# Performance work log

Measured on AMD Instinct MI355X. Metric: run time of the kernel, lower is better.

The kernel has to match this reference:

```python
import jax, jax.numpy as jnp
import numpy as np

# ---- layer config (yolov3, layer_no=2) ----
STRIDE = 8
N_CLASSES = 80
IGNORE_TH = 0.7
ANCHORS_PX = np.array([[10,13],[16,30],[33,23],[30,61],[62,45],[59,119],[116,90],[156,198],[373,326]], np.float32)
ALL_ANCHORS = ANCHORS_PX / STRIDE          # [9,2] in grid units
ANCHOR_ID_LO, ANCHOR_ID_HI = 0, 2          # anchor_mask[2] = [0,1,2]
ANCHORS = ALL_ANCHORS[ANCHOR_ID_LO:ANCHOR_ID_HI+1]  # [3,2]
NA = 3
NC = N_CLASSES + 5

B, IN_CH, NG, NBOX = 16, 256, 76, 50


def _safe_log(p):
    # emulate torch BCE's log clamp at -100; eps stops 0*inf -> nan
    return jnp.maximum(jnp.log(jnp.maximum(p, 1e-12)), -100.0)


def _bce_sum(p, t, w=None):
    l = -(t * _safe_log(p) + (1.0 - t) * _safe_log(1.0 - p))
    if w is not None:
        l = l * w
    return l.sum()


def setup_inputs() -> dict:
    key = jax.random.key(0)
    k1, k2, k3, k4, k5 = jax.random.split(key, 5)
    xin = jax.random.normal(k1, (B, IN_CH, NG, NG), jnp.float32)
    cls = jax.random.randint(k2, (B, NBOX, 1), 0, N_CLASSES).astype(jnp.float32)
    cxy = jax.random.uniform(k3, (B, NBOX, 2), jnp.float32, 0.02, 0.98)
    wh = jax.random.uniform(k4, (B, NBOX, 2), jnp.float32, 0.02, 0.40)
    labels = jnp.concatenate([cls, cxy, wh], axis=-1)  # [B,N,5]
    W = jax.random.normal(k5, (NA * NC, IN_CH), jnp.float32) * 0.02  # 1x1 conv
    b = jnp.zeros((NA * NC,), jnp.float32)
    return {"xin": xin, "labels": labels, "W": W, "b": b}


def _yolo_loss(xin, labels, W, b):
    nB, _, nG, _ = xin.shape
    anchors = jnp.asarray(ANCHORS, xin.dtype)          # [3,2]
    all_anchors = jnp.asarray(ALL_ANCHORS, xin.dtype)  # [9,2]

    # 1x1 conv -> [B, A, G, G, C]
    x = jnp.einsum('bchw,oc->bohw', xin, W) + b[None, :, None, None]
    x = x.reshape(nB, NA, NC, nG, nG).transpose(0, 1, 3, 4, 2)

    xy = jax.nn.sigmoid(x[..., :2])
    wh = x[..., 2:4]
    conf_cls = jax.nn.sigmoid(x[..., 4:])  # [B,A,G,G,1+ncls]

    gy, gx = jnp.meshgrid(jnp.arange(nG, dtype=x.dtype), jnp.arange(nG, dtype=x.dtype), indexing='ij')
    pred_boxes = jnp.stack([
        xy[..., 0] + gx,
        xy[..., 1] + gy,
        jnp.exp(wh[..., 0]) * anchors[:, 0][None, :, None, None],
        jnp.exp(wh[..., 1]) * anchors[:, 1][None, :, None, None]], axis=-1)  # [B,A,G,G,4]

    # ---- ground truth ----
    valid = labels.sum(-1) > 0                     # [B,N]
    gt_cls = labels[..., 0].astype(jnp.int32)
    gt = labels[..., 1:] * nG                      # [B,N,4] cx,cy,w,h in grid units
    gt_x, gt_y, gt_w, gt_h = gt[..., 0], gt[..., 1], gt[..., 2], gt[..., 3]
    gi = jnp.floor(gt_x).astype(jnp.int32)
    gj = jnp.floor(gt_y).astype(jnp.int32)

    # best anchor per gt: wh-IoU vs all 9 anchors (centered at origin)
    inter_a = jnp.minimum(gt_w[..., None], all_anchors[:, 0]) * jnp.minimum(gt_h[..., None], all_anchors[:, 1])
    union_a = gt_w[..., None] * gt_h[..., None] + all_anchors[:, 0] * all_anchors[:, 1] - inter_a
    best = jnp.argmax(inter_a / union_a, axis=-1)  # [B,N]
    in_mask = (best >= ANCHOR_ID_LO) & (best <= ANCHOR_ID_HI)
    a = jnp.where(in_mask, best % 3, -1)           # [B,N]

    # all-pairs IoU: pred boxes vs gt boxes (ignore mask)
    pb = pred_boxes.reshape(nB, -1, 4)             # [B,M,4], M = A*G*G
    pa_area = pb[..., 2] * pb[..., 3]
    gt_area = gt_w * gt_h
    tl = jnp.maximum(pb[:, :, None, :2] - pb[:, :, None, 2:] / 2, gt[:, None, :, :2] - gt[:, None, :, 2:] / 2)
    br = jnp.minimum(pb[:, :, None, :2] + pb[:, :, None, 2:] / 2, gt[:, None, :, :2] + gt[:, None, :, 2:] / 2)
    inter = jnp.prod(br - tl, -1) * jnp.all(tl < br, -1)
    iou = inter / (pa_area[:, :, None] + gt_area[:, None, :] - inter)
    iou = jnp.where(valid[:, None, :], iou, 0.0)
    best_iou = iou.max(-1)                         # [B,M]
    has_boxes = valid.any(-1)
    obj_mask = jnp.where(has_boxes[:, None], best_iou <= IGNORE_TH, True).reshape(nB, NA, nG, nG)

    # ---- scatter target assignment ----
    assign = valid & (a >= 0)
    a_safe = jnp.clip(a, 0, NA - 1)
    aw = anchors[a_safe, 0]
    ah = anchors[a_safe, 1]
    tvec = jnp.concatenate([
        (gt_x - jnp.floor(gt_x))[..., None],
        (gt_y - jnp.floor(gt_y))[..., None],
        jnp.log(gt_w / aw + 1e-16)[..., None],
        jnp.log(gt_h / ah + 1e-16)[..., None],
        jnp.ones_like(gt_x)[..., None],
        jax.nn.one_hot(gt_cls, N_CLASSES, dtype=x.dtype)], axis=-1)  # [B,N,NC]
    sval = 2.0 - gt_w * gt_h / (nG * nG)

    bf = jnp.broadcast_to(jnp.arange(nB)[:, None], a.shape).reshape(-1)
    af = jnp.where(assign, a_safe, NA).reshape(-1)  # NA is OOB -> dropped
    jf = gj.reshape(-1)
    if_ = gi.reshape(-1)

    target = jnp.zeros((nB, NA, nG, nG, NC), x.dtype).at[bf, af, jf, if_].set(tvec.reshape(-1, NC), mode='drop')
    scale = jnp.zeros((nB, NA, nG, nG), x.dtype).at[bf, af, jf, if_].set(sval.reshape(-1), mode='drop')
    obj_mask = obj_mask.at[bf, af, jf, if_].set(True, mode='drop')
    noobj = jnp.zeros((nB, NA, nG, nG), bool).at[bf, af, jf, if_].set(True, mode='drop')

    # ---- losses ----
    nm = noobj.astype(x.dtype)[..., None]
    p_obj = conf_cls[..., 0] * obj_mask
    t_obj = target[..., 4] * obj_mask
    p_xy = xy * nm
    t_xy = target[..., :2] * nm
    p_wh = wh * nm
    t_wh = target[..., 2:4] * nm
    p_cls = conf_cls[..., 1:] * nm
    t_cls = target[..., 5:] * nm
    sc = scale[..., None]

    loss_xy = _bce_sum(p_xy, t_xy, sc)
    rs = jnp.sqrt(sc)
    loss_wh = 0.5 * jnp.sum((p_wh * rs - t_wh * rs) ** 2)
    loss_obj = _bce_sum(p_obj, t_obj)
    loss_cls = _bce_sum(p_cls, t_cls)
    loss = loss_xy + loss_wh + loss_obj + loss_cls
    return jnp.stack([loss, loss_xy, loss_wh, loss_obj, loss_cls])


def reference(xin, labels, W, b):
    return _yolo_loss(xin, labels, W, b)
```

## Files before the change

### kernel.cpp

```cpp
#include <hip/hip_runtime.h>
#include <math.h>

#define NB    16
#define NAg   3
#define NCg   85
#define NCLS  80
#define NGg   76
#define NSp   (NGg*NGg)
#define NBOX  50
#define INCH  256
#define SPB   256
#define GBLK  ((NSp + SPB - 1) / SPB)
#define GXDIM (GBLK + NBOX)
#define TOTBLK (GXDIM * NB)

#define ACC_OFF  0
#define HAS_OFF  32
#define DONE_OFF 96
#define WT_OFF   128
#define GB_OFF   (WT_OFF + 16384)
#define GA_OFF   (GB_OFF + 25600)
#define GI_OFF   (GA_OFF + 25600)

__device__ __constant__ float c_AW[9] = {1.25f,2.0f,4.125f,3.75f,7.75f,7.375f,14.5f,19.5f,46.625f};
__device__ __constant__ float c_AH[9] = {1.625f,3.75f,2.875f,7.625f,5.625f,14.875f,11.25f,24.75f,40.75f};

__device__ __forceinline__ float safe_log(float p) {
    return fmaxf(logf(fmaxf(p, 1e-12f)), -100.0f);
}
__device__ __forceinline__ float sigm(float x) {
    return 1.0f / (1.0f + expf(-x));
}

__global__ __launch_bounds__(256) void k_labels(
    const float* __restrict__ labels, const float* __restrict__ W,
    float* __restrict__ Wt, float* __restrict__ gbox, float* __restrict__ gaux,
    int* __restrict__ gint, int* __restrict__ hasAny, float* __restrict__ acc,
    int* __restrict__ done)
{
    const int b = blockIdx.x, tid = threadIdx.x;
    const int t = b * 256 + tid;

    {
        const int c = t >> 4, f = t & 15;
        Wt[t] = (f < 15) ? W[((f / 5) * NCg + (f % 5)) * INCH + c] : 0.f;
    }
    if (b == 0 && tid < 8)  acc[tid] = 0.f;
    if (b == 0 && tid == 8) *done = 0;

    int valid = 0;
    if (tid < NBOX) {
        const int bt = b * NBOX + tid;
        const float* L = labels + (size_t)bt * 5;
        const float l0 = L[0], l1 = L[1], l2 = L[2], l3 = L[3], l4 = L[4];
        valid = (l0 + l1 + l2 + l3 + l4) > 0.f;

        const float gx = l1 * NGg, gy = l2 * NGg, gw = l3 * NGg, gh = l4 * NGg;

        int best = 0; float brr = -1.f;
#pragma unroll
        for (int k = 0; k < 9; k++) {
            float inter = fminf(gw, c_AW[k]) * fminf(gh, c_AH[k]);
            float uni   = gw*gh + c_AW[k]*c_AH[k] - inter;
            float r     = inter / uni;
            if (r > brr) { brr = r; best = k; }
        }
        const int a = (best <= 2) ? best : -1;
        const int assign = valid && (a >= 0);
        const int a_safe = a < 0 ? 0 : (a > 2 ? 2 : a);

        const int gi = (int)floorf(gx), gj = (int)floorf(gy);
        const int inb = (gi >= 0) && (gi < NGg) && (gj >= 0) && (gj < NGg);
        const int cell = (assign && inb) ? (a * NSp + gj * NGg + gi) : -1;

        float* gb = gbox + (size_t)bt * 8;
        gb[0] = gx - gw * 0.5f;
        gb[1] = gy - gh * 0.5f;
        gb[2] = gx + gw * 0.5f;
        gb[3] = gy + gh * 0.5f;
        gb[4] = valid ? gw * gh : -1.f;
        gb[5] = __int_as_float(cell);

        float* ga = gaux + (size_t)bt * 8;
        ga[0] = gx - floorf(gx);
        ga[1] = gy - floorf(gy);
        ga[2] = logf(gw / c_AW[a_safe] + 1e-16f);
        ga[3] = logf(gh / c_AH[a_safe] + 1e-16f);
        ga[4] = 2.f - gw * gh / (float)NSp;

        gint[bt*2 + 0] = cell;
        gint[bt*2 + 1] = (int)l0;
    }
    if (tid < 64) {
        const unsigned long long m = __ballot(valid != 0);
        if (tid == 0) hasAny[b] = (m != 0ULL) ? 1 : 0;
    }
}

__global__ __launch_bounds__(256) void k_mega(
    const float* __restrict__ xin, const float* __restrict__ Wt,
    const float* __restrict__ W, const float* __restrict__ bias,
    const float* __restrict__ gbox, const float* __restrict__ gaux,
    const int* __restrict__ gint, const int* __restrict__ hasAny,
    float* __restrict__ acc, int* __restrict__ done, float* __restrict__ out)
{
    __shared__ __align__(16) float smem[15364];

    const int bx  = blockIdx.x;
    const int b   = blockIdx.y;
    const int tid = threadIdx.x;

    if (bx < GBLK) {
        float (*part)[15][SPB] = (float (*)[15][SPB])smem;
        float* wred = smem + 4 * 15 * SPB;

        const int w  = tid >> 6, l = tid & 63;
        const int wu = __builtin_amdgcn_readfirstlane(w);
        const int pb = bx * SPB;

        float4 ac[15];
#pragma unroll
        for (int f = 0; f < 15; ++f) ac[f] = make_float4(0.f,0.f,0.f,0.f);

        const float* xp = xin + ((size_t)b * INCH + (wu << 6)) * NSp + pb + 4*l;
        const float* wp = Wt + ((wu << 6) << 4);

        if (pb + SPB <= NSp) {
            for (int c0 = 0; c0 < 64; c0 += 8) {
                float4 v[8];
#pragma unroll
                for (int k = 0; k < 8; ++k)
                    v[k] = *(const float4*)(xp + (size_t)(c0 + k) * NSp);
#pragma unroll
                for (int k = 0; k < 8; ++k) {
                    const float* wr = wp + ((c0 + k) << 4);
#pragma unroll
                    for (int f = 0; f < 15; ++f) {
                        const float wv = wr[f];
                        ac[f].x += wv * v[k].x;  ac[f].y += wv * v[k].y;
                        ac[f].z += wv * v[k].z;  ac[f].w += wv * v[k].w;
                    }
                }
            }
        } else {
            const bool lv = (pb + 4*l) < NSp;
            const float4 z = make_float4(0.f,0.f,0.f,0.f);
            for (int c0 = 0; c0 < 64; c0 += 8) {
                float4 v[8];
#pragma unroll
                for (int k = 0; k < 8; ++k)
                    v[k] = lv ? *(const float4*)(xp + (size_t)(c0 + k) * NSp) : z;
#pragma unroll
                for (int k = 0; k < 8; ++k) {
                    const float* wr = wp + ((c0 + k) << 4);
#pragma unroll
                    for (int f = 0; f < 15; ++f) {
                        const float wv = wr[f];
                        ac[f].x += wv * v[k].x;  ac[f].y += wv * v[k].y;
                        ac[f].z += wv * v[k].z;  ac[f].w += wv * v[k].w;
                    }
                }
            }
        }

#pragma unroll
        for (int f = 0; f < 15; ++f)
            *(float4*)&part[w][f][4*l] = ac[f];
        __syncthreads();

        float lsum = 0.f;
        const int p = pb + tid;
        if (p < NSp) {
            float xv[15];
#pragma unroll
            for (int f = 0; f < 15; ++f)
                xv[f] = part[0][f][tid] + part[1][f][tid]
                      + part[2][f][tid] + part[3][f][tid];

            const int sy = p / NGg;
            const int sx = p - sy * NGg;
            const float gxf = (float)sx, gyf = (float)sy;

            float pbx0[3], pby0[3], pbx1[3], pby1[3], pa[3], cf[3];
#pragma unroll
            for (int a = 0; a < 3; ++a) {
                const float px = sigm(xv[a*5+0] + bias[a*NCg+0]) + gxf;
                const float py = sigm(xv[a*5+1] + bias[a*NCg+1]) + gyf;
                const float pw = expf(xv[a*5+2] + bias[a*NCg+2]) * c_AW[a];
                const float ph = expf(xv[a*5+3] + bias[a*NCg+3]) * c_AH[a];
                cf[a]   = sigm(xv[a*5+4] + bias[a*NCg+4]);
                pbx0[a] = px - pw * 0.5f;  pby0[a] = py - ph * 0.5f;
                pbx1[a] = px + pw * 0.5f;  pby1[a] = py + ph * 0.5f;
                pa[a]   = pw * ph;
            }

            int mask = 0;
            const float* gb = gbox + (size_t)b * NBOX * 8;
            for (int n = 0; n < NBOX; ++n) {
                const float bx0 = gb[n*8+0], by0 = gb[n*8+1];
                const float bx1 = gb[n*8+2], by1 = gb[n*8+3];
                const float gar = gb[n*8+4];
                const int cell  = __float_as_int(gb[n*8+5]);
                const int d = cell - p;
                if (d == 0)       mask |= 8;
                if (d == NSp)     mask |= 16;
                if (d == 2*NSp)   mask |= 32;
                if (gar >= 0.f) {
#pragma unroll
                    for (int a = 0; a < 3; ++a) {
                        const float tlx = fmaxf(pbx0[a], bx0);
                        const float tly = fmaxf(pby0[a], by0);
                        const float brx = fminf(pbx1[a], bx1);
                        const float bry = fminf(pby1[a], by1);
                        const float dx = brx - tlx, dy = bry - tly;
                        const float inter = (dx > 0.f && dy > 0.f) ? dx * dy : 0.f;
                        if (inter > 0.7f * (pa[a] + gar - inter)) mask |= (1 << a);
                    }
                }
            }

            const bool hasB = hasAny[b] != 0;
#pragma unroll
            for (int a = 0; a < 3; ++a) {
                const bool ex = (mask & (1 << a)) != 0;
                const bool as = (mask & (8 << a)) != 0;
                const bool maskpre = hasB ? (!ex) : true;
                if (maskpre || as) {
                    const float c = cf[a];
                    lsum += as ? -safe_log(c) : -safe_log(1.f - c);
                }
            }
        }

#pragma unroll
        for (int off = 32; off > 0; off >>= 1) lsum += __shfl_down(lsum, off);
        if ((tid & 63) == 0) wred[tid >> 6] = lsum;
        __syncthreads();
        if (tid == 0) atomicAdd(&acc[2], wred[0] + wred[1] + wred[2] + wred[3]);

    } else {
        int*    scell = (int*)smem;
        float4* col4  = (float4*)(smem + 64);
        float*  xsh   = smem + 64 + 256;
        float*  sacc  = smem + 64 + 256 + 96;

        const int n = bx - GBLK;
        const int t = b * NBOX + n;

        if (tid < NBOX) scell[tid] = gint[(b * NBOX + tid) * 2];
        __syncthreads();

        const int cell = scell[n];
        bool win = (cell >= 0);
        if (win)
            for (int n2 = n + 1; n2 < NBOX; ++n2)
                if (scell[n2] == cell) { win = false; break; }

        if (win) {
            const int a = cell / NSp, s = cell % NSp;
            const int o0 = a * NCg;

            ((float*)col4)[tid] = xin[((size_t)b * INCH + tid) * NSp + s];
            if (tid < 3) sacc[tid] = 0.f;
            __syncthreads();

            const int wid = tid >> 6, lane = tid & 63;
            for (int o = wid; o < NCg; o += 4) {
                const float4 wv = *(const float4*)&W[(size_t)(o0 + o) * INCH + lane * 4];
                const float4 cv = col4[lane];
                float p = wv.x*cv.x + wv.y*cv.y + wv.z*cv.z + wv.w*cv.w;
                for (int off = 32; off; off >>= 1) p += __shfl_down(p, off);
                if (lane == 0) xsh[o] = p + bias[o0 + o];
            }
            __syncthreads();

            if (tid < NCg) {
                const float* ga = gaux + (size_t)t * 8;
                const float sval = ga[4];
                const int gcls = gint[t*2 + 1];
                float val = xsh[tid];
                float term; int slot;
                if (tid < 2) {
                    float tgt = ga[tid];
                    float p = sigm(val);
                    term = -(tgt * safe_log(p) + (1.f - tgt) * safe_log(1.f - p)) * sval;
                    slot = 0;
                } else if (tid < 4) {
                    float tgt = ga[tid];
                    float d = val - tgt;
                    term = 0.5f * sval * d * d;
                    slot = 1;
                } else if (tid == 4) {
                    term = 0.f; slot = 2;
                } else {
                    float tgt = ((tid - 5) == gcls) ? 1.f : 0.f;
                    float p = sigm(val);
                    term = -(tgt * safe_log(p) + (1.f - tgt) * safe_log(1.f - p));
                    slot = 2;
                }
                atomicAdd(&sacc[slot], term);
            }
            __syncthreads();
            if (tid == 0) {
                atomicAdd(&acc[0], sacc[0]);
                atomicAdd(&acc[1], sacc[1]);
                atomicAdd(&acc[3], sacc[2]);
            }
        }
    }

    __syncthreads();
    if (tid == 0) {
        __threadfence();
        const int v = atomicAdd(done, 1);
        if (v == TOTBLK - 1) {
            const float xy = atomicAdd(&acc[0], 0.f);
            const float wh = atomicAdd(&acc[1], 0.f);
            const float ob = atomicAdd(&acc[2], 0.f);
            const float cl = atomicAdd(&acc[3], 0.f);
            out[0] = xy + wh + ob + cl;
            out[1] = xy; out[2] = wh; out[3] = ob; out[4] = cl;
        }
    }
}

extern "C" void kernel_launch(void* const* d_in, const int* in_sizes, int n_in,
                              void* d_out, int out_size, void* d_ws, size_t ws_size,
                              hipStream_t stream)
{
    const float* xin    = (const float*)d_in[0];
    const float* labels = (const float*)d_in[1];
    const float* W      = (const float*)d_in[2];
    const float* bias   = (const float*)d_in[3];

    char* ws = (char*)d_ws;
    float* acc    = (float*)(ws + ACC_OFF);
    int*   hasAny = (int*)  (ws + HAS_OFF);
    int*   done   = (int*)  (ws + DONE_OFF);
    float* Wt     = (float*)(ws + WT_OFF);
    float* gbox   = (float*)(ws + GB_OFF);
    float* gaux   = (float*)(ws + GA_OFF);
    int*   gint   = (int*)  (ws + GI_OFF);
    float* out    = (float*)d_out;

    k_labels<<<16, 256, 0, stream>>>(labels, W, Wt, gbox, gaux, gint, hasAny, acc, done);

    k_mega<<<dim3(GXDIM, NB), 256, 0, stream>>>(xin, Wt, W, bias, gbox, gaux,
                                                gint, hasAny, acc, done, out);
}
```

Measured before the change: 205.2 us.

## Fold per-box target blocks into spatial blocks via strided loop

Removes the 50 extra per-GT-box blocks per batch from the grid. Each spatial conv/objectness block now also handles a strided subset of the GT boxes after its main work, reusing its shared memory. This shrinks the grid and the completion-counter traffic, but adds serial per-box work and extra barriers to the tail of the spatial blocks.

Measured after the change: 196.6 us. 1.04x faster.

```diff
diff --git a/kernel.cpp b/kernel.cpp
--- a/kernel.cpp
+++ b/kernel.cpp
@@ -11,8 +11,7 @@
 #define INCH  256
 #define SPB   256
 #define GBLK  ((NSp + SPB - 1) / SPB)
-#define GXDIM (GBLK + NBOX)
-#define TOTBLK (GXDIM * NB)
+#define TOTBLK (GBLK * NB)
 
 #define ACC_OFF  0
 #define HAS_OFF  32
@@ -97,159 +96,152 @@
     }
 }
 
-__global__ __launch_bounds__(256) void k_mega(
+__global__ __launch_bounds__(256) void k_main(
     const float* __restrict__ xin, const float* __restrict__ Wt,
     const float* __restrict__ W, const float* __restrict__ bias,
     const float* __restrict__ gbox, const float* __restrict__ gaux,
     const int* __restrict__ gint, const int* __restrict__ hasAny,
     float* __restrict__ acc, int* __restrict__ done, float* __restrict__ out)
 {
-    __shared__ __align__(16) float smem[15364];
+    __shared__ float part[4][15][SPB];
+    __shared__ float wred[4];
 
     const int bx  = blockIdx.x;
     const int b   = blockIdx.y;
     const int tid = threadIdx.x;
-
-    if (bx < GBLK) {
-        float (*part)[15][SPB] = (float (*)[15][SPB])smem;
-        float* wred = smem + 4 * 15 * SPB;
-
-        const int w  = tid >> 6, l = tid & 63;
-        const int wu = __builtin_amdgcn_readfirstlane(w);
-        const int pb = bx * SPB;
-
-        float4 ac[15];
-#pragma unroll
-        for (int f = 0; f < 15; ++f) ac[f] = make_float4(0.f,0.f,0.f,0.f);
-
-        const float* xp = xin + ((size_t)b * INCH + (wu << 6)) * NSp + pb + 4*l;
-        const float* wp = Wt + ((wu << 6) << 4);
-
-        if (pb + SPB <= NSp) {
-            for (int c0 = 0; c0 < 64; c0 += 8) {
-                float4 v[8];
-#pragma unroll
-                for (int k = 0; k < 8; ++k)
-                    v[k] = *(const float4*)(xp + (size_t)(c0 + k) * NSp);
-#pragma unroll
-                for (int k = 0; k < 8; ++k) {
-                    const float* wr = wp + ((c0 + k) << 4);
-#pragma unroll
-                    for (int f = 0; f < 15; ++f) {
-                        const float wv = wr[f];
-                        ac[f].x += wv * v[k].x;  ac[f].y += wv * v[k].y;
-                        ac[f].z += wv * v[k].z;  ac[f].w += wv * v[k].w;
-                    }
+    const int w   = tid >> 6, l = tid & 63;
+    const int wu  = __builtin_amdgcn_readfirstlane(w);
+    const int pb  = bx * SPB;
+
+    float4 ac[15];
+#pragma unroll
+    for (int f = 0; f < 15; ++f) ac[f] = make_float4(0.f,0.f,0.f,0.f);
+
+    const float* xp = xin + ((size_t)b * INCH + (wu << 6)) * NSp + pb + 4*l;
+    const float* wp = Wt + ((wu << 6) << 4);
+
+    if (pb + SPB <= NSp) {
+        for (int c0 = 0; c0 < 64; c0 += 8) {
+            float4 v[8];
+#pragma unroll
+            for (int k = 0; k < 8; ++k)
+                v[k] = *(const float4*)(xp + (size_t)(c0 + k) * NSp);
+#pragma unroll
+            for (int k = 0; k < 8; ++k) {
+                const float* wr = wp + ((c0 + k) << 4);
+#pragma unroll
+                for (int f = 0; f < 15; ++f) {
+                    const float wv = wr[f];
+                    ac[f].x += wv * v[k].x;  ac[f].y += wv * v[k].y;
+                    ac[f].z += wv * v[k].z;  ac[f].w += wv * v[k].w;
                 }
             }
-        } else {
-            const bool lv = (pb + 4*l) < NSp;
-            const float4 z = make_float4(0.f,0.f,0.f,0.f);
-            for (int c0 = 0; c0 < 64; c0 += 8) {
-                float4 v[8];
-#pragma unroll
-                for (int k = 0; k < 8; ++k)
-                    v[k] = lv ? *(const float4*)(xp + (size_t)(c0 + k) * NSp) : z;
-#pragma unroll
-                for (int k = 0; k < 8; ++k) {
-                    const float* wr = wp + ((c0 + k) << 4);
-#pragma unroll
-                    for (int f = 0; f < 15; ++f) {
-                        const float wv = wr[f];
-                        ac[f].x += wv * v[k].x;  ac[f].y += wv * v[k].y;
-                        ac[f].z += wv * v[k].z;  ac[f].w += wv * v[k].w;
-                    }
+        }
+    } else {
+        const bool lv = (pb + 4*l) < NSp;
+        const float4 z = make_float4(0.f,0.f,0.f,0.f);
+        for (int c0 = 0; c0 < 64; c0 += 8) {
+            float4 v[8];
+#pragma unroll
+            for (int k = 0; k < 8; ++k)
+                v[k] = lv ? *(const float4*)(xp + (size_t)(c0 + k) * NSp) : z;
+#pragma unroll
+            for (int k = 0; k < 8; ++k) {
+                const float* wr = wp + ((c0 + k) << 4);
+#pragma unroll
+                for (int f = 0; f < 15; ++f) {
+                    const float wv = wr[f];
+                    ac[f].x += wv * v[k].x;  ac[f].y += wv * v[k].y;
+                    ac[f].z += wv * v[k].z;  ac[f].w += wv * v[k].w;
                 }
             }
         }
-
+    }
+
+#pragma unroll
+    for (int f = 0; f < 15; ++f)
+        *(float4*)&part[w][f][4*l] = ac[f];
+    __syncthreads();
+
+    float lsum = 0.f;
+    const int p = pb + tid;
+    if (p < NSp) {
+        float xv[15];
 #pragma unroll
         for (int f = 0; f < 15; ++f)
-            *(float4*)&part[w][f][4*l] = ac[f];
-        __syncthreads();
-
-        float lsum = 0.f;
-        const int p = pb + tid;
-        if (p < NSp) {
-            float xv[15];
-#pragma unroll
-            for (int f = 0; f < 15; ++f)
-                xv[f] = part[0][f][tid] + part[1][f][tid]
-                      + part[2][f][tid] + part[3][f][tid];
-
-            const int sy = p / NGg;
-            const int sx = p - sy * NGg;
-            const float gxf = (float)sx, gyf = (float)sy;
-
-            float pbx0[3], pby0[3], pbx1[3], pby1[3], pa[3], cf[3];
-#pragma unroll
-            for (int a = 0; a < 3; ++a) {
-                const float px = sigm(xv[a*5+0] + bias[a*NCg+0]) + gxf;
-                const float py = sigm(xv[a*5+1] + bias[a*NCg+1]) + gyf;
-                const float pw = expf(xv[a*5+2] + bias[a*NCg+2]) * c_AW[a];
-                const float ph = expf(xv[a*5+3] + bias[a*NCg+3]) * c_AH[a];
-                cf[a]   = sigm(xv[a*5+4] + bias[a*NCg+4]);
-                pbx0[a] = px - pw * 0.5f;  pby0[a] = py - ph * 0.5f;
-                pbx1[a] = px + pw * 0.5f;  pby1[a] = py + ph * 0.5f;
-                pa[a]   = pw * ph;
-            }
-
-            int mask = 0;
-            const float* gb = gbox + (size_t)b * NBOX * 8;
-            for (int n = 0; n < NBOX; ++n) {
-                const float bx0 = gb[n*8+0], by0 = gb[n*8+1];
-                const float bx1 = gb[n*8+2], by1 = gb[n*8+3];
-                const float gar = gb[n*8+4];
-                const int cell  = __float_as_int(gb[n*8+5]);
-                const int d = cell - p;
-                if (d == 0)       mask |= 8;
-                if (d == NSp)     mask |= 16;
-                if (d == 2*NSp)   mask |= 32;
-                if (gar >= 0.f) {
-#pragma unroll
-                    for (int a = 0; a < 3; ++a) {
-                        const float tlx = fmaxf(pbx0[a], bx0);
-                        const float tly = fmaxf(pby0[a], by0);
-                        const float brx = fminf(pbx1[a], bx1);
-                        const float bry = fminf(pby1[a], by1);
-                        const float dx = brx - tlx, dy = bry - tly;
-                        const float inter = (dx > 0.f && dy > 0.f) ? dx * dy : 0.f;
-                        if (inter > 0.7f * (pa[a] + gar - inter)) mask |= (1 << a);
-                    }
+            xv[f] = part[0][f][tid] + part[1][f][tid]
+                  + part[2][f][tid] + part[3][f][tid];
+
+        const int sy = p / NGg;
+        const int sx = p - sy * NGg;
+        const float gxf = (float)sx, gyf = (float)sy;
+
+        float pbx0[3], pby0[3], pbx1[3], pby1[3], pa[3], cf[3];
+#pragma unroll
+        for (int a = 0; a < 3; ++a) {
+            const float px = sigm(xv[a*5+0] + bias[a*NCg+0]) + gxf;
+            const float py = sigm(xv[a*5+1] + bias[a*NCg+1]) + gyf;
+            const float pw = expf(xv[a*5+2] + bias[a*NCg+2]) * c_AW[a];
+            const float ph = expf(xv[a*5+3] + bias[a*NCg+3]) * c_AH[a];
+            cf[a]   = sigm(xv[a*5+4] + bias[a*NCg+4]);
+            pbx0[a] = px - pw * 0.5f;  pby0[a] = py - ph * 0.5f;
+            pbx1[a] = px + pw * 0.5f;  pby1[a] = py + ph * 0.5f;
+            pa[a]   = pw * ph;
+        }
+
+        int mask = 0;
+        const float* gb = gbox + (size_t)b * NBOX * 8;
+        for (int n = 0; n < NBOX; ++n) {
+            const float bx0 = gb[n*8+0], by0 = gb[n*8+1];
+            const float bx1 = gb[n*8+2], by1 = gb[n*8+3];
+            const float gar = gb[n*8+4];
+            const int cell  = __float_as_int(gb[n*8+5]);
+            const int d = cell - p;
+            if (d == 0)       mask |= 8;
+            if (d == NSp)     mask |= 16;
+            if (d == 2*NSp)   mask |= 32;
+            if (gar >= 0.f) {
+#pragma unroll
+                for (int a = 0; a < 3; ++a) {
+                    const float tlx = fmaxf(pbx0[a], bx0);
+                    const float tly = fmaxf(pby0[a], by0);
+                    const float brx = fminf(pbx1[a], bx1);
+                    const float bry = fminf(pby1[a], by1);
+                    const float dx = brx - tlx, dy = bry - tly;
+                    const float inter = (dx > 0.f && dy > 0.f) ? dx * dy : 0.f;
+                    if (inter > 0.7f * (pa[a] + gar - inter)) mask |= (1 << a);
                 }
             }
-
-            const bool hasB = hasAny[b] != 0;
-#pragma unroll
-            for (int a = 0; a < 3; ++a) {
-                const bool ex = (mask & (1 << a)) != 0;
-                const bool as = (mask & (8 << a)) != 0;
-                const bool maskpre = hasB ? (!ex) : true;
-                if (maskpre || as) {
-                    const float c = cf[a];
-                    lsum += as ? -safe_log(c) : -safe_log(1.f - c);
-                }
-            }
-        }
-
-#pragma unroll
-        for (int off = 32; off > 0; off >>= 1) lsum += __shfl_down(lsum, off);
-        if ((tid & 63) == 0) wred[tid >> 6] = lsum;
-        __syncthreads();
-        if (tid == 0) atomicAdd(&acc[2], wred[0] + wred[1] + wred[2] + wred[3]);
-
-    } else {
-        int*    scell = (int*)smem;
-        float4* col4  = (float4*)(smem + 64);
-        float*  xsh   = smem + 64 + 256;
-        float*  sacc  = smem + 64 + 256 + 96;
-
-        const int n = bx - GBLK;
-        const int t = b * NBOX + n;
-
-        if (tid < NBOX) scell[tid] = gint[(b * NBOX + tid) * 2];
-        __syncthreads();
-
+        }
+
+        const bool hasB = hasAny[b] != 0;
+#pragma unroll
+        for (int a = 0; a < 3; ++a) {
+            const bool ex = (mask & (1 << a)) != 0;
+            const bool as = (mask & (8 << a)) != 0;
+            const bool maskpre = hasB ? (!ex) : true;
+            if (maskpre || as) {
+                const float c = cf[a];
+                lsum += as ? -safe_log(c) : -safe_log(1.f - c);
+            }
+        }
+    }
+
+#pragma unroll
+    for (int off = 32; off > 0; off >>= 1) lsum += __shfl_down(lsum, off);
+    if (l == 0) wred[w] = lsum;
+    __syncthreads();
+    if (tid == 0) atomicAdd(&acc[2], wred[0] + wred[1] + wred[2] + wred[3]);
+
+    int*   scell = (int*)&part[0][0][0];
+    float* colv  = &part[0][1][0];
+    float* xsh   = &part[0][2][0];
+    float* sacc  = &part[0][3][0];
+
+    if (tid < NBOX) scell[tid] = gint[(b * NBOX + tid) * 2];
+    __syncthreads();
+
+    for (int n = bx; n < NBOX; n += GBLK) {
         const int cell = scell[n];
         bool win = (cell >= 0);
         if (win)
@@ -259,18 +251,18 @@
         if (win) {
             const int a = cell / NSp, s = cell % NSp;
             const int o0 = a * NCg;
-
-            ((float*)col4)[tid] = xin[((size_t)b * INCH + tid) * NSp + s];
+            const int t  = b * NBOX + n;
+
+            colv[tid] = xin[((size_t)b * INCH + tid) * NSp + s];
             if (tid < 3) sacc[tid] = 0.f;
             __syncthreads();
 
-            const int wid = tid >> 6, lane = tid & 63;
-            for (int o = wid; o < NCg; o += 4) {
-                const float4 wv = *(const float4*)&W[(size_t)(o0 + o) * INCH + lane * 4];
-                const float4 cv = col4[lane];
-                float p = wv.x*cv.x + wv.y*cv.y + wv.z*cv.z + wv.w*cv.w;
-                for (int off = 32; off; off >>= 1) p += __shfl_down(p, off);
-                if (lane == 0) xsh[o] = p + bias[o0 + o];
+            for (int o = w; o < NCg; o += 4) {
+                const float4 wv = *(const float4*)&W[(size_t)(o0 + o) * INCH + l * 4];
+                const float4 cv = *(const float4*)&colv[l * 4];
+                float pr = wv.x*cv.x + wv.y*cv.y + wv.z*cv.z + wv.w*cv.w;
+                for (int off = 32; off; off >>= 1) pr += __shfl_down(pr, off);
+                if (l == 0) xsh[o] = pr + bias[o0 + o];
             }
             __syncthreads();
 
@@ -282,8 +274,8 @@
                 float term; int slot;
                 if (tid < 2) {
                     float tgt = ga[tid];
-                    float p = sigm(val);
-                    term = -(tgt * safe_log(p) + (1.f - tgt) * safe_log(1.f - p)) * sval;
+                    float pp = sigm(val);
+                    term = -(tgt * safe_log(pp) + (1.f - tgt) * safe_log(1.f - pp)) * sval;
                     slot = 0;
                 } else if (tid < 4) {
                     float tgt = ga[tid];
@@ -294,8 +286,8 @@
                     term = 0.f; slot = 2;
                 } else {
                     float tgt = ((tid - 5) == gcls) ? 1.f : 0.f;
-                    float p = sigm(val);
-                    term = -(tgt * safe_log(p) + (1.f - tgt) * safe_log(1.f - p));
+                    float pp = sigm(val);
+                    term = -(tgt * safe_log(pp) + (1.f - tgt) * safe_log(1.f - pp));
                     slot = 2;
                 }
                 atomicAdd(&sacc[slot], term);
@@ -306,10 +298,10 @@
                 atomicAdd(&acc[1], sacc[1]);
                 atomicAdd(&acc[3], sacc[2]);
             }
-        }
-    }
-
-    __syncthreads();
+            __syncthreads();
+        }
+    }
+
     if (tid == 0) {
         __threadfence();
         const int v = atomicAdd(done, 1);
@@ -345,6 +337,6 @@
 
     k_labels<<<16, 256, 0, stream>>>(labels, W, Wt, gbox, gaux, gint, hasAny, acc, done);
 
-    k_mega<<<dim3(GXDIM, NB), 256, 0, stream>>>(xin, Wt, W, bias, gbox, gaux,
-                                                gint, hasAny, acc, done, out);
-}
+    k_main<<<dim3(GBLK, NB), 256, 0, stream>>>(xin, Wt, W, bias, gbox, gaux,
+                                               gint, hasAny, acc, done, out);
+}
```

## Split conv work per block into 2 position halves x 2 channel halves

Applied to the files above, without the earlier changes.

Each wave now handles 128 positions (2 per lane, float2 loads) and half of the 256 input channels, where before it handled all 256 positions (float4 per lane) and a quarter of the channels. The partial-sum buffer in LDS shrinks from four slices to two, which cuts LDS use and the cross-wave reduction work. In exchange, each lane issues narrower global loads and has a longer channel loop. The per-lane accumulator registers drop from 60 to 30 floats, which may allow higher occupancy.

After: 209.2 us. Within noise of the previous version (+2.0%).

```diff
diff --git a/kernel.cpp b/kernel.cpp
--- a/kernel.cpp
+++ b/kernel.cpp
@@ -104,7 +104,7 @@
     const int* __restrict__ gint, const int* __restrict__ hasAny,
     float* __restrict__ acc, int* __restrict__ done, float* __restrict__ out)
 {
-    __shared__ __align__(16) float smem[15364];
+    __shared__ __align__(16) float smem[2*15*SPB + 4];
 
     const int bx  = blockIdx.x;
     const int b   = blockIdx.y;
@@ -112,60 +112,45 @@
 
     if (bx < GBLK) {
         float (*part)[15][SPB] = (float (*)[15][SPB])smem;
-        float* wred = smem + 4 * 15 * SPB;
+        float* wred = smem + 2*15*SPB;
 
         const int w  = tid >> 6, l = tid & 63;
         const int wu = __builtin_amdgcn_readfirstlane(w);
-        const int pb = bx * SPB;
-
-        float4 ac[15];
-#pragma unroll
-        for (int f = 0; f < 15; ++f) ac[f] = make_float4(0.f,0.f,0.f,0.f);
-
-        const float* xp = xin + ((size_t)b * INCH + (wu << 6)) * NSp + pb + 4*l;
-        const float* wp = Wt + ((wu << 6) << 4);
-
-        if (pb + SPB <= NSp) {
-            for (int c0 = 0; c0 < 64; c0 += 8) {
-                float4 v[8];
+        const int posHalf = wu >> 1;
+        const int chBase  = (wu & 1) << 7;
+        const int pb  = bx * SPB;
+        const int pOff = (posHalf << 7) + 2*l;
+        const int p0  = pb + pOff;
+        const bool live = p0 < NSp;
+
+        float2 a2[15];
+#pragma unroll
+        for (int f = 0; f < 15; ++f) a2[f] = make_float2(0.f, 0.f);
+
+        const float* xp = xin + ((size_t)b * INCH + chBase) * NSp + p0;
+        const float* wp = Wt + (chBase << 4);
+
+        if (live) {
+            for (int c0 = 0; c0 < 128; c0 += 8) {
+                float2 v[8];
 #pragma unroll
                 for (int k = 0; k < 8; ++k)
-                    v[k] = *(const float4*)(xp + (size_t)(c0 + k) * NSp);
+                    v[k] = *(const float2*)(xp + (size_t)(c0 + k) * NSp);
 #pragma unroll
                 for (int k = 0; k < 8; ++k) {
                     const float* wr = wp + ((c0 + k) << 4);
 #pragma unroll
                     for (int f = 0; f < 15; ++f) {
                         const float wv = wr[f];
-                        ac[f].x += wv * v[k].x;  ac[f].y += wv * v[k].y;
-                        ac[f].z += wv * v[k].z;  ac[f].w += wv * v[k].w;
+                        a2[f].x += wv * v[k].x;
+                        a2[f].y += wv * v[k].y;
                     }
                 }
             }
-        } else {
-            const bool lv = (pb + 4*l) < NSp;
-            const float4 z = make_float4(0.f,0.f,0.f,0.f);
-            for (int c0 = 0; c0 < 64; c0 += 8) {
-                float4 v[8];
-#pragma unroll
-                for (int k = 0; k < 8; ++k)
-                    v[k] = lv ? *(const float4*)(xp + (size_t)(c0 + k) * NSp) : z;
-#pragma unroll
-                for (int k = 0; k < 8; ++k) {
-                    const float* wr = wp + ((c0 + k) << 4);
-#pragma unroll
-                    for (int f = 0; f < 15; ++f) {
-                        const float wv = wr[f];
-                        ac[f].x += wv * v[k].x;  ac[f].y += wv * v[k].y;
-                        ac[f].z += wv * v[k].z;  ac[f].w += wv * v[k].w;
-                    }
-                }
-            }
-        }
-
+        }
 #pragma unroll
         for (int f = 0; f < 15; ++f)
-            *(float4*)&part[w][f][4*l] = ac[f];
+            *(float2*)&part[wu & 1][f][pOff] = a2[f];
         __syncthreads();
 
         float lsum = 0.f;
@@ -174,8 +159,7 @@
             float xv[15];
 #pragma unroll
             for (int f = 0; f < 15; ++f)
-                xv[f] = part[0][f][tid] + part[1][f][tid]
-                      + part[2][f][tid] + part[3][f][tid];
+                xv[f] = part[0][f][tid] + part[1][f][tid];
 
             const int sy = p / NGg;
             const int sx = p - sy * NGg;
@@ -234,7 +218,7 @@
 
 #pragma unroll
         for (int off = 32; off > 0; off >>= 1) lsum += __shfl_down(lsum, off);
-        if ((tid & 63) == 0) wred[tid >> 6] = lsum;
+        if (l == 0) wred[w] = lsum;
         __syncthreads();
         if (tid == 0) atomicAdd(&acc[2], wred[0] + wred[1] + wred[2] + wred[3]);
 
@@ -282,8 +266,8 @@
                 float term; int slot;
                 if (tid < 2) {
                     float tgt = ga[tid];
-                    float p = sigm(val);
-                    term = -(tgt * safe_log(p) + (1.f - tgt) * safe_log(1.f - p)) * sval;
+                    float pp = sigm(val);
+                    term = -(tgt * safe_log(pp) + (1.f - tgt) * safe_log(1.f - pp)) * sval;
                     slot = 0;
                 } else if (tid < 4) {
                     float tgt = ga[tid];
@@ -294,8 +278,8 @@
                     term = 0.f; slot = 2;
                 } else {
                     float tgt = ((tid - 5) == gcls) ? 1.f : 0.f;
-                    float p = sigm(val);
-                    term = -(tgt * safe_log(p) + (1.f - tgt) * safe_log(1.f - p));
+                    float pp = sigm(val);
+                    term = -(tgt * safe_log(pp) + (1.f - tgt) * safe_log(1.f - pp));
                     slot = 2;
                 }
                 atomicAdd(&sacc[slot], term);
```
